# Performance work log

Measured on AMD Instinct MI355X. Metric: run time of the kernel, lower is better.

## Reference

```python
import jax, jax.numpy as jnp
import numpy as np

L, D, DFF, H, B, S = 6, 1024, 4096, 16, 4, 512
DK = D // H
EPS = 1e-6


def setup_inputs() -> dict:
    key = jax.random.key(0)
    ks = jax.random.split(key, 20)
    sc = 0.02
    n = jax.random.normal
    return {
        "x": n(ks[0], (B, S, D), jnp.float32),
        "Wq": n(ks[1], (L, D, D)) * sc, "bq": jnp.zeros((L, D)),
        "Wk": n(ks[2], (L, D, D)) * sc, "bk": jnp.zeros((L, D)),
        "Wv": n(ks[3], (L, D, D)) * sc, "bv": jnp.zeros((L, D)),
        "Wo": n(ks[4], (L, D, D)) * sc, "bo": jnp.zeros((L, D)),
        "W1": n(ks[5], (L, D, DFF)) * sc, "b1": jnp.zeros((L, DFF)),
        "W2": n(ks[6], (L, DFF, D)) * sc, "b2": jnp.zeros((L, D)),
        "ln1_a": jnp.ones((L, D)), "ln1_b": jnp.zeros((L, D)),
        "ln2_a": jnp.ones((L, D)), "ln2_b": jnp.zeros((L, D)),
        "norm_a": jnp.ones((D,)), "norm_b": jnp.zeros((D,)),
    }


def _ln(x, a, b):
    # custom LayerNorm: uses sample std (ddof=1, like torch.std) and (std + eps)
    m = x.mean(-1, keepdims=True)
    s = jnp.std(x, axis=-1, ddof=1, keepdims=True)
    return a * (x - m) / (s + EPS) + b


def reference(x, Wq, bq, Wk, bk, Wv, bv, Wo, bo, W1, b1, W2, b2,
              ln1_a, ln1_b, ln2_a, ln2_b, norm_a, norm_b):
    inv = 1.0 / jnp.sqrt(jnp.float32(DK))
    for l in range(L):
        # --- self-attention sublayer (pre-norm, residual) ---
        h = _ln(x, ln1_a[l], ln1_b[l])
        q = (h @ Wq[l] + bq[l]).reshape(B, S, H, DK)
        k = (h @ Wk[l] + bk[l]).reshape(B, S, H, DK)
        v = (h @ Wv[l] + bv[l]).reshape(B, S, H, DK)
        scores = jnp.einsum('bqhd,bkhd->bhqk', q, k) * inv
        p = jax.nn.softmax(scores, axis=-1)
        o = jnp.einsum('bhqk,bkhd->bqhd', p, v).reshape(B, S, D)
        x = x + (o @ Wo[l] + bo[l])
        # --- feed-forward sublayer ---
        h = _ln(x, ln2_a[l], ln2_b[l])
        x = x + (jax.nn.relu(h @ W1[l] + b1[l]) @ W2[l] + b2[l])
    return _ln(x, norm_a, norm_b)
```

## Files before the change

kernel.cpp:

```cpp
#include <hip/hip_runtime.h>
#include <hip/hip_bf16.h>

typedef __hip_bfloat16 bf16;
typedef __bf16 bf16x8 __attribute__((ext_vector_type(8)));
typedef float f32x4 __attribute__((ext_vector_type(4)));

static constexpr int L_ = 6, D_ = 1024, DFF_ = 4096, H_ = 16, B_ = 4, S_ = 512, DK_ = 64;
static constexpr int N_ = B_ * S_;

#define GLOAD_LDS(gp, lp) __builtin_amdgcn_global_load_lds( \
    (const __attribute__((address_space(1))) void*)(gp),    \
    (__attribute__((address_space(3))) void*)(lp), 16, 0, 0)

__global__ void transpose_cast(const float* __restrict__ in, bf16* __restrict__ out,
                               int K, int M, long zin, long zout) {
    const float* ip = in + (size_t)blockIdx.z * zin;
    bf16* op = out + (size_t)blockIdx.z * zout;
    __shared__ float t[32][33];
    int m0 = blockIdx.x * 32, k0 = blockIdx.y * 32;
    int tx = threadIdx.x, ty = threadIdx.y;
    #pragma unroll
    for (int i = 0; i < 32; i += 8)
        t[ty + i][tx] = ip[(size_t)(k0 + ty + i) * M + m0 + tx];
    __syncthreads();
    #pragma unroll
    for (int i = 0; i < 32; i += 8)
        op[(size_t)(m0 + ty + i) * K + k0 + tx] = __float2bfloat16(t[tx][ty + i]);
}

__global__ void pack_qkv_bias(const float* __restrict__ bq, const float* __restrict__ bk,
                              const float* __restrict__ bv, float* __restrict__ out) {
    int t = blockIdx.x * 256 + threadIdx.x;
    int l = t / (3 * D_), c = t % (3 * D_);
    float v = c < D_ ? bq[l * D_ + c] : (c < 2 * D_ ? bk[l * D_ + c - D_] : bv[l * D_ + c - 2 * D_]);
    out[t] = v;
}

template <typename OutT>
__global__ __launch_bounds__(256) void ln_kernel(const float* __restrict__ x,
                                                 const float* __restrict__ ga,
                                                 const float* __restrict__ gb,
                                                 OutT* __restrict__ out) {
    int row = blockIdx.x;
    float4 v = ((const float4*)(x + (size_t)row * D_))[threadIdx.x];
    float s = v.x + v.y + v.z + v.w;
    float q = v.x * v.x + v.y * v.y + v.z * v.z + v.w * v.w;
    #pragma unroll
    for (int m = 1; m < 64; m <<= 1) { s += __shfl_xor(s, m, 64); q += __shfl_xor(q, m, 64); }
    __shared__ float ps[4], pq[4];
    int wid = threadIdx.x >> 6;
    if ((threadIdx.x & 63) == 0) { ps[wid] = s; pq[wid] = q; }
    __syncthreads();
    s = ps[0] + ps[1] + ps[2] + ps[3];
    q = pq[0] + pq[1] + pq[2] + pq[3];
    float mean = s * (1.0f / D_);
    float var = (q - (float)D_ * mean * mean) * (1.0f / (D_ - 1));
    var = var < 0.f ? 0.f : var;
    float rstd = 1.0f / (sqrtf(var) + 1e-6f);
    int c = threadIdx.x * 4;
    float xv[4] = {v.x, v.y, v.z, v.w};
    #pragma unroll
    for (int r = 0; r < 4; r++) {
        float o = ga[c + r] * (xv[r] - mean) * rstd + gb[c + r];
        if constexpr (__hip_internal::is_same<OutT, float>::value)
            out[(size_t)row * D_ + c + r] = o;
        else
            out[(size_t)row * D_ + c + r] = __float2bfloat16(o);
    }
}

__device__ inline void swz_tiles(int& ntile, int& mtile) {
    unsigned o = blockIdx.y * gridDim.x + blockIdx.x;
    if (gridDim.z == 1) {
        unsigned nwg = gridDim.x * gridDim.y;
        unsigned q = nwg >> 3, r = nwg & 7;
        unsigned xcd = o & 7, j = o >> 3;
        o = (xcd < r ? xcd * (q + 1) : r * (q + 1) + (xcd - r) * q) + j;
    }
    ntile = o % gridDim.x;
    mtile = o / gridDim.x;
}

enum { EPI_RELU = 2, EPI_ATOMIC = 4 };

template <int BM, int BN, int EPI, int SPLITK = 1>
__global__ __launch_bounds__(256) void gemm_bt(
    const bf16* __restrict__ A, int lda,
    const bf16* __restrict__ Bt, int ldb,
    const float* __restrict__ bias,
    void* __restrict__ Cv, int ldc,
    int K) {
    constexpr int BK = 64;
    constexpr int WM = BM / 2, WN = BN / 2;
    constexpr int FM = WM / 16, FN = WN / 16;
    constexpr int IA = BM / 32;
    constexpr int IB = BN / 32;
    __shared__ __align__(16) bf16 As[2][BM * BK];
    __shared__ __align__(16) bf16 Bs[2][BN * BK];
    const int tid = threadIdx.x, wid = tid >> 6, lane = tid & 63;
    const int kz = (SPLITK > 1) ? blockIdx.z : 0;
    int ntile, mtile;
    swz_tiles(ntile, mtile);
    const int m0 = mtile * BM, n0 = ntile * BN;
    const int wm = (wid >> 1) * WM, wn = (wid & 1) * WN;
    const int fr = lane & 15, fg = lane >> 4;
    const int sr = lane >> 3;
    const int c8s = (lane & 7) ^ (sr & 7);
    const int Kc = K / SPLITK;
    const int kbeg = kz * Kc, kend = kbeg + Kc;

    auto stage = [&](int buf, int k0) {
        #pragma unroll
        for (int i = 0; i < IA; i++) {
            int inst = wid * IA + i;
            const bf16* gp = A + (size_t)(m0 + inst * 8 + sr) * lda + k0 + c8s * 8;
            GLOAD_LDS(gp, &As[buf][inst * 512]);
        }
        #pragma unroll
        for (int i = 0; i < IB; i++) {
            int inst = wid * IB + i;
            const bf16* gp = Bt + (size_t)(n0 + inst * 8 + sr) * ldb + k0 + c8s * 8;
            GLOAD_LDS(gp, &Bs[buf][inst * 512]);
        }
    };

    f32x4 acc[FM][FN] = {};
    stage(0, kbeg);
    __syncthreads();
    int cur = 0;
    for (int k0 = kbeg; k0 < kend; k0 += BK) {
        if (k0 + BK < kend) stage(cur ^ 1, k0 + BK);
        #pragma unroll
        for (int kk = 0; kk < 2; kk++) {
            const int cs = ((kk << 2) + fg) ^ (fr & 7);
            bf16x8 af[FM], bfr[FN];
            #pragma unroll
            for (int i = 0; i < FM; i++)
                af[i] = *(const bf16x8*)&As[cur][(wm + i * 16 + fr) * BK + cs * 8];
            #pragma unroll
            for (int j = 0; j < FN; j++)
                bfr[j] = *(const bf16x8*)&Bs[cur][(wn + j * 16 + fr) * BK + cs * 8];
            #pragma unroll
            for (int i = 0; i < FM; i++)
                #pragma unroll
                for (int j = 0; j < FN; j++)
                    acc[i][j] = __builtin_amdgcn_mfma_f32_16x16x32_bf16(af[i], bfr[j], acc[i][j], 0, 0, 0);
        }
        __syncthreads();
        cur ^= 1;
    }
    #pragma unroll
    for (int i = 0; i < FM; i++) {
        #pragma unroll
        for (int j = 0; j < FN; j++) {
            int rr = m0 + wm + i * 16 + (lane >> 4) * 4;
            int cc = n0 + wn + j * 16 + (lane & 15);
            float bv = bias[cc];
            #pragma unroll
            for (int r = 0; r < 4; r++) {
                float v = acc[i][j][r];
                if constexpr (EPI == EPI_RELU) {
                    bf16* C = (bf16*)Cv;
                    float o = v + bv;
                    C[(size_t)(rr + r) * ldc + cc] = __float2bfloat16(o > 0.f ? o : 0.f);
                } else {
                    float* C = (float*)Cv;
                    atomicAdd(&C[(size_t)(rr + r) * ldc + cc], v + (kz == 0 ? bv : 0.f));
                }
            }
        }
    }
}

__global__ __launch_bounds__(256) void gemm_qkv(
    const bf16* __restrict__ A, const bf16* __restrict__ Bt, const float* __restrict__ bias,
    bf16* __restrict__ qb, bf16* __restrict__ kb, bf16* __restrict__ vT) {
    constexpr int BM = 128, BN = 128, BK = 64;
    constexpr int WM = 64, WN = 64, FM = 4, FN = 4;
    __shared__ __align__(16) bf16 As[2][BM * BK];
    __shared__ __align__(16) bf16 Bs[2][BN * BK];
    const int tid = threadIdx.x, wid = tid >> 6, lane = tid & 63;
    int ntile, mtile;
    swz_tiles(ntile, mtile);
    const int m0 = mtile * BM, n0 = ntile * BN;
    const int wm = (wid >> 1) * WM, wn = (wid & 1) * WN;
    const int fr = lane & 15, fg = lane >> 4;
    const int sr = lane >> 3;
    const int c8s = (lane & 7) ^ (sr & 7);

    auto stage = [&](int buf, int k0) {
        #pragma unroll
        for (int i = 0; i < 4; i++) {
            int inst = wid * 4 + i;
            const bf16* gp = A + (size_t)(m0 + inst * 8 + sr) * D_ + k0 + c8s * 8;
            GLOAD_LDS(gp, &As[buf][inst * 512]);
        }
        #pragma unroll
        for (int i = 0; i < 4; i++) {
            int inst = wid * 4 + i;
            const bf16* gp = Bt + (size_t)(n0 + inst * 8 + sr) * D_ + k0 + c8s * 8;
            GLOAD_LDS(gp, &Bs[buf][inst * 512]);
        }
    };

    f32x4 acc[FM][FN] = {};
    stage(0, 0);
    __syncthreads();
    int cur = 0;
    for (int k0 = 0; k0 < D_; k0 += BK) {
        if (k0 + BK < D_) stage(cur ^ 1, k0 + BK);
        #pragma unroll
        for (int kk = 0; kk < 2; kk++) {
            const int cs = ((kk << 2) + fg) ^ (fr & 7);
            bf16x8 af[FM], bfr[FN];
            #pragma unroll
            for (int i = 0; i < FM; i++)
                af[i] = *(const bf16x8*)&As[cur][(wm + i * 16 + fr) * BK + cs * 8];
            #pragma unroll
            for (int j = 0; j < FN; j++)
                bfr[j] = *(const bf16x8*)&Bs[cur][(wn + j * 16 + fr) * BK + cs * 8];
            #pragma unroll
            for (int i = 0; i < FM; i++)
                #pragma unroll
                for (int j = 0; j < FN; j++)
                    acc[i][j] = __builtin_amdgcn_mfma_f32_16x16x32_bf16(af[i], bfr[j], acc[i][j], 0, 0, 0);
        }
        __syncthreads();
        cur ^= 1;
    }
    #pragma unroll
    for (int i = 0; i < FM; i++) {
        #pragma unroll
        for (int j = 0; j < FN; j++) {
            int rr = m0 + wm + i * 16 + (lane >> 4) * 4;
            int cc = n0 + wn + j * 16 + (lane & 15);
            float bv = bias[cc];
            #pragma unroll
            for (int r = 0; r < 4; r++) {
                float v = acc[i][j][r] + bv;
                if (cc < D_) {
                    qb[(size_t)(rr + r) * D_ + cc] = __float2bfloat16(v);
                } else if (cc < 2 * D_) {
                    kb[(size_t)(rr + r) * D_ + cc - D_] = __float2bfloat16(v);
                } else {
                    vT[((size_t)(rr >> 9) * D_ + cc - 2 * D_) * S_ + ((rr & 511) + r)] = __float2bfloat16(v);
                }
            }
        }
    }
}

__global__ __launch_bounds__(256) void flash_attn(
    const bf16* __restrict__ qb, const bf16* __restrict__ kb, const bf16* __restrict__ vT,
    bf16* __restrict__ ob) {
    __shared__ __align__(16) bf16 P[4][16 * 64];
    const int lane = threadIdx.x & 63, wid = threadIdx.x >> 6;
    const int b = blockIdx.y >> 4, h = blockIdx.y & 15;
    const int q0 = blockIdx.x * 64 + wid * 16;
    const int fr = lane & 15, fg = lane >> 4;
    bf16* Pw = &P[wid][0];

    const bf16* qrow = qb + ((size_t)(b * S_ + q0 + fr)) * D_ + h * DK_ + fg * 8;
    bf16x8 aq0 = *(const bf16x8*)(qrow);
    bf16x8 aq1 = *(const bf16x8*)(qrow + 32);

    f32x4 accO[4] = {};
    float mrow[4] = {-1e30f, -1e30f, -1e30f, -1e30f};
    float lrow[4] = {};

    for (int kv0 = 0; kv0 < S_; kv0 += 64) {
        f32x4 s[4] = {};
        #pragma unroll
        for (int j = 0; j < 4; j++) {
            const bf16* krow = kb + ((size_t)(b * S_ + kv0 + j * 16 + fr)) * D_ + h * DK_ + fg * 8;
            bf16x8 bk0 = *(const bf16x8*)(krow);
            bf16x8 bk1 = *(const bf16x8*)(krow + 32);
            s[j] = __builtin_amdgcn_mfma_f32_16x16x32_bf16(aq0, bk0, s[j], 0, 0, 0);
            s[j] = __builtin_amdgcn_mfma_f32_16x16x32_bf16(aq1, bk1, s[j], 0, 0, 0);
        }
        float tmax[4], alpha[4], rs[4];
        #pragma unroll
        for (int r = 0; r < 4; r++) {
            #pragma unroll
            for (int j = 0; j < 4; j++) s[j][r] *= 0.125f;
            tmax[r] = fmaxf(fmaxf(s[0][r], s[1][r]), fmaxf(s[2][r], s[3][r]));
            #pragma unroll
            for (int m = 1; m < 16; m <<= 1) tmax[r] = fmaxf(tmax[r], __shfl_xor(tmax[r], m, 64));
            float mn = fmaxf(mrow[r], tmax[r]);
            alpha[r] = __expf(mrow[r] - mn);
            mrow[r] = mn;
            rs[r] = 0.f;
        }
        #pragma unroll
        for (int j = 0; j < 4; j++) {
            #pragma unroll
            for (int r = 0; r < 4; r++) {
                float p = __expf(s[j][r] - mrow[r]);
                rs[r] += p;
                int q = fg * 4 + r;
                int col = (j * 16 + fr) ^ ((q & 7) << 3);
                Pw[q * 64 + col] = __float2bfloat16(p);
            }
        }
        #pragma unroll
        for (int r = 0; r < 4; r++) {
            #pragma unroll
            for (int m = 1; m < 16; m <<= 1) rs[r] += __shfl_xor(rs[r], m, 64);
            lrow[r] = lrow[r] * alpha[r] + rs[r];
            #pragma unroll
            for (int j = 0; j < 4; j++) accO[j][r] *= alpha[r];
        }
        #pragma unroll
        for (int ks = 0; ks < 2; ks++) {
            int kk = (ks * 32 + fg * 8) ^ ((fr & 7) << 3);
            bf16x8 ap = *(const bf16x8*)&Pw[fr * 64 + kk];
            #pragma unroll
            for (int j = 0; j < 4; j++) {
                const bf16* vrow = vT + ((size_t)(b * D_) + h * DK_ + j * 16 + fr) * S_ + kv0 + ks * 32 + fg * 8;
                bf16x8 bv = *(const bf16x8*)(vrow);
                accO[j] = __builtin_amdgcn_mfma_f32_16x16x32_bf16(ap, bv, accO[j], 0, 0, 0);
            }
        }
    }
    #pragma unroll
    for (int j = 0; j < 4; j++) {
        #pragma unroll
        for (int r = 0; r < 4; r++) {
            int q = q0 + fg * 4 + r;
            int d = h * DK_ + j * 16 + fr;
            ob[(size_t)(b * S_ + q) * D_ + d] = __float2bfloat16(accO[j][r] / lrow[r]);
        }
    }
}

extern "C" void kernel_launch(void* const* d_in, const int* in_sizes, int n_in,
                              void* d_out, int out_size, void* d_ws, size_t ws_size,
                              hipStream_t stream) {
    (void)in_sizes; (void)n_in; (void)out_size;
    const float* x    = (const float*)d_in[0];
    const float* Wq   = (const float*)d_in[1];
    const float* pbq  = (const float*)d_in[2];
    const float* Wk   = (const float*)d_in[3];
    const float* pbk  = (const float*)d_in[4];
    const float* Wv   = (const float*)d_in[5];
    const float* pbv  = (const float*)d_in[6];
    const float* Wo   = (const float*)d_in[7];
    const float* pbo  = (const float*)d_in[8];
    const float* W1   = (const float*)d_in[9];
    const float* pb1  = (const float*)d_in[10];
    const float* W2   = (const float*)d_in[11];
    const float* pb2  = (const float*)d_in[12];
    const float* l1a  = (const float*)d_in[13];
    const float* l1b  = (const float*)d_in[14];
    const float* l2a  = (const float*)d_in[15];
    const float* l2b  = (const float*)d_in[16];
    const float* nrma = (const float*)d_in[17];
    const float* nrmb = (const float*)d_in[18];

    char* ws = (char*)d_ws;
    size_t off = 0;
    auto alloc = [&](size_t bytes) { void* p = ws + off; off += (bytes + 255) & ~(size_t)255; return p; };
    float* xf  = (float*)alloc((size_t)N_ * D_ * 4);
    bf16* hbuf = (bf16*)alloc((size_t)N_ * D_ * 2);
    bf16* qbuf = (bf16*)alloc((size_t)N_ * D_ * 2);
    bf16* kbuf = (bf16*)alloc((size_t)N_ * D_ * 2);
    bf16* vT   = (bf16*)alloc((size_t)B_ * D_ * S_ * 2);
    bf16* obuf = (bf16*)alloc((size_t)N_ * D_ * 2);
    float* qkvb = (float*)alloc((size_t)L_ * 3 * D_ * 4);
    bf16* mid  = (bf16*)alloc((size_t)N_ * DFF_ * 2);
    const size_t szDD = (size_t)D_ * D_, szDF = (size_t)D_ * DFF_;
    size_t wtFull = (3 * L_ * szDD + L_ * szDD + 2 * L_ * szDF) * 2;
    size_t wtLayer = (4 * szDD + 2 * szDF) * 2;
    bool full = (off + wtFull) <= ws_size;
    bf16* WT = (bf16*)alloc(full ? wtFull : wtLayer);

    pack_qkv_bias<<<L_ * 3 * D_ / 256, 256, 0, stream>>>(pbq, pbk, pbv, qkvb);

    bf16 *Wqkv0, *WoT0, *W1T0, *W2T0;
    dim3 tb(32, 8);
    if (full) {
        Wqkv0 = WT;
        WoT0  = WT + 3 * L_ * szDD;
        W1T0  = WoT0 + L_ * szDD;
        W2T0  = W1T0 + L_ * szDF;
        transpose_cast<<<dim3(D_ / 32, D_ / 32, L_), tb, 0, stream>>>(Wq, Wqkv0, D_, D_, szDD, 3 * szDD);
        transpose_cast<<<dim3(D_ / 32, D_ / 32, L_), tb, 0, stream>>>(Wk, Wqkv0 + szDD, D_, D_, szDD, 3 * szDD);
        transpose_cast<<<dim3(D_ / 32, D_ / 32, L_), tb, 0, stream>>>(Wv, Wqkv0 + 2 * szDD, D_, D_, szDD, 3 * szDD);
        transpose_cast<<<dim3(D_ / 32, D_ / 32, L_), tb, 0, stream>>>(Wo, WoT0, D_, D_, szDD, szDD);
        transpose_cast<<<dim3(DFF_ / 32, D_ / 32, L_), tb, 0, stream>>>(W1, W1T0, D_, DFF_, szDF, szDF);
        transpose_cast<<<dim3(D_ / 32, DFF_ / 32, L_), tb, 0, stream>>>(W2, W2T0, DFF_, D_, szDF, szDF);
    } else {
        Wqkv0 = WT; WoT0 = WT + 3 * szDD; W1T0 = WoT0 + szDD; W2T0 = W1T0 + szDF;
    }

    hipMemcpyAsync(xf, x, (size_t)N_ * D_ * 4, hipMemcpyDeviceToDevice, stream);

    for (int l = 0; l < L_; l++) {
        const bf16 *WqkvT, *WoT, *W1T, *W2T;
        if (full) {
            WqkvT = Wqkv0 + (size_t)l * 3 * szDD;
            WoT = WoT0 + l * szDD; W1T = W1T0 + l * szDF; W2T = W2T0 + l * szDF;
        } else {
            transpose_cast<<<dim3(D_ / 32, D_ / 32, 1), tb, 0, stream>>>(Wq + l * szDD, Wqkv0, D_, D_, 0, 0);
            transpose_cast<<<dim3(D_ / 32, D_ / 32, 1), tb, 0, stream>>>(Wk + l * szDD, Wqkv0 + szDD, D_, D_, 0, 0);
            transpose_cast<<<dim3(D_ / 32, D_ / 32, 1), tb, 0, stream>>>(Wv + l * szDD, Wqkv0 + 2 * szDD, D_, D_, 0, 0);
            transpose_cast<<<dim3(D_ / 32, D_ / 32, 1), tb, 0, stream>>>(Wo + l * szDD, WoT0, D_, D_, 0, 0);
            transpose_cast<<<dim3(DFF_ / 32, D_ / 32, 1), tb, 0, stream>>>(W1 + l * szDF, W1T0, D_, DFF_, 0, 0);
            transpose_cast<<<dim3(D_ / 32, DFF_ / 32, 1), tb, 0, stream>>>(W2 + l * szDF, W2T0, DFF_, D_, 0, 0);
            WqkvT = Wqkv0; WoT = WoT0; W1T = W1T0; W2T = W2T0;
        }

        ln_kernel<bf16><<<N_, 256, 0, stream>>>(xf, l1a + l * D_, l1b + l * D_, hbuf);
        gemm_qkv<<<dim3(3 * D_ / 128, N_ / 128, 1), 256, 0, stream>>>(
            hbuf, WqkvT, qkvb + (size_t)l * 3 * D_, qbuf, kbuf, vT);
        flash_attn<<<dim3(S_ / 64, B_ * H_), 256, 0, stream>>>(qbuf, kbuf, vT, obuf);
        gemm_bt<128, 64, EPI_ATOMIC, 2><<<dim3(D_ / 64, N_ / 128, 2), 256, 0, stream>>>(
            obuf, D_, WoT, D_, pbo + l * D_, xf, D_, D_);

        ln_kernel<bf16><<<N_, 256, 0, stream>>>(xf, l2a + l * D_, l2b + l * D_, hbuf);
        gemm_bt<128, 128, EPI_RELU><<<dim3(DFF_ / 128, N_ / 128, 1), 256, 0, stream>>>(
            hbuf, D_, W1T, D_, pb1 + l * DFF_, mid, DFF_, D_);
        gemm_bt<128, 128, EPI_ATOMIC, 4><<<dim3(D_ / 128, N_ / 128, 4), 256, 0, stream>>>(
            mid, DFF_, W2T, DFF_, pb2 + l * D_, xf, D_, DFF_);
    }

    ln_kernel<float><<<N_, 256, 0, stream>>>(xf, nrma, nrmb, (float*)d_out);
}
```

Measured before the change: 1.162 ms.

## Use 256x128 8-wave GEMM, split-K partial buffers, fuse residual reduction with LayerNorm

Replaces the 256-thread GEMMs with one 512-thread kernel using 256x128 tiles for QKV, W1, Wo and W2. Split-K GEMMs now write partial sums to a workspace instead of doing float atomics. A new reduce_ln kernel sums the partials into the residual and applies the next LayerNorm in the same pass, replacing the separate ln_kernel launches. This removes atomic contention and one pass over the activations, at the cost of a 4x N*D fp32 workspace and fewer, larger blocks per GEMM.

```diff
diff --git a/kernel.cpp b/kernel.cpp
--- a/kernel.cpp
+++ b/kernel.cpp
@@ -69,6 +69,44 @@
     }
 }
 
+template <int S, typename OutT>
+__global__ __launch_bounds__(256) void reduce_ln(
+    const float* __restrict__ parts, long sK, float* __restrict__ xf,
+    const float* __restrict__ ga, const float* __restrict__ gb, OutT* __restrict__ out) {
+    int row = blockIdx.x;
+    float4 v = ((const float4*)(xf + (size_t)row * D_))[threadIdx.x];
+    #pragma unroll
+    for (int s = 0; s < S; s++) {
+        float4 p = ((const float4*)(parts + (size_t)s * sK + (size_t)row * D_))[threadIdx.x];
+        v.x += p.x; v.y += p.y; v.z += p.z; v.w += p.w;
+    }
+    ((float4*)(xf + (size_t)row * D_))[threadIdx.x] = v;
+    float sum = v.x + v.y + v.z + v.w;
+    float q = v.x * v.x + v.y * v.y + v.z * v.z + v.w * v.w;
+    #pragma unroll
+    for (int m = 1; m < 64; m <<= 1) { sum += __shfl_xor(sum, m, 64); q += __shfl_xor(q, m, 64); }
+    __shared__ float ps[4], pq[4];
+    int wid = threadIdx.x >> 6;
+    if ((threadIdx.x & 63) == 0) { ps[wid] = sum; pq[wid] = q; }
+    __syncthreads();
+    sum = ps[0] + ps[1] + ps[2] + ps[3];
+    q = pq[0] + pq[1] + pq[2] + pq[3];
+    float mean = sum * (1.0f / D_);
+    float var = (q - (float)D_ * mean * mean) * (1.0f / (D_ - 1));
+    var = var < 0.f ? 0.f : var;
+    float rstd = 1.0f / (sqrtf(var) + 1e-6f);
+    int c = threadIdx.x * 4;
+    float xv[4] = {v.x, v.y, v.z, v.w};
+    #pragma unroll
+    for (int r = 0; r < 4; r++) {
+        float o = ga[c + r] * (xv[r] - mean) * rstd + gb[c + r];
+        if constexpr (__hip_internal::is_same<OutT, float>::value)
+            out[(size_t)row * D_ + c + r] = o;
+        else
+            out[(size_t)row * D_ + c + r] = __float2bfloat16(o);
+    }
+}
+
 __device__ inline void swz_tiles(int& ntile, int& mtile) {
     unsigned o = blockIdx.y * gridDim.x + blockIdx.x;
     if (gridDim.z == 1) {
@@ -81,20 +119,19 @@
     mtile = o / gridDim.x;
 }
 
-enum { EPI_RELU = 2, EPI_ATOMIC = 4 };
-
-template <int BM, int BN, int EPI, int SPLITK = 1>
-__global__ __launch_bounds__(256) void gemm_bt(
+enum { EPI_RELU = 0, EPI_PART = 1, EPI_QKV = 2 };
+
+template <int EPI, int SPLITK = 1>
+__global__ __launch_bounds__(512) void gemm8(
     const bf16* __restrict__ A, int lda,
     const bf16* __restrict__ Bt, int ldb,
     const float* __restrict__ bias,
-    void* __restrict__ Cv, int ldc,
-    int K) {
-    constexpr int BK = 64;
-    constexpr int WM = BM / 2, WN = BN / 2;
-    constexpr int FM = WM / 16, FN = WN / 16;
-    constexpr int IA = BM / 32;
-    constexpr int IB = BN / 32;
+    void* __restrict__ Cv, int ldc, long sK, int K,
+    bf16* __restrict__ qb, bf16* __restrict__ kb, bf16* __restrict__ vT) {
+    constexpr int BM = 256, BN = 128, BK = 64;
+    constexpr int FM = 4, FN = 4;
+    constexpr int IA = BM / 64;
+    constexpr int IB = BN / 64;
     __shared__ __align__(16) bf16 As[2][BM * BK];
     __shared__ __align__(16) bf16 Bs[2][BN * BK];
     const int tid = threadIdx.x, wid = tid >> 6, lane = tid & 63;
@@ -102,7 +139,7 @@
     int ntile, mtile;
     swz_tiles(ntile, mtile);
     const int m0 = mtile * BM, n0 = ntile * BN;
-    const int wm = (wid >> 1) * WM, wn = (wid & 1) * WN;
+    const int wm = (wid >> 1) * 64, wn = (wid & 1) * 64;
     const int fr = lane & 15, fg = lane >> 4;
     const int sr = lane >> 3;
     const int c8s = (lane & 7) ^ (sr & 7);
@@ -163,87 +200,18 @@
                     bf16* C = (bf16*)Cv;
                     float o = v + bv;
                     C[(size_t)(rr + r) * ldc + cc] = __float2bfloat16(o > 0.f ? o : 0.f);
+                } else if constexpr (EPI == EPI_PART) {
+                    float* C = (float*)Cv;
+                    C[(size_t)kz * sK + (size_t)(rr + r) * ldc + cc] = v + (kz == 0 ? bv : 0.f);
                 } else {
-                    float* C = (float*)Cv;
-                    atomicAdd(&C[(size_t)(rr + r) * ldc + cc], v + (kz == 0 ? bv : 0.f));
-                }
-            }
-        }
-    }
-}
-
-__global__ __launch_bounds__(256) void gemm_qkv(
-    const bf16* __restrict__ A, const bf16* __restrict__ Bt, const float* __restrict__ bias,
-    bf16* __restrict__ qb, bf16* __restrict__ kb, bf16* __restrict__ vT) {
-    constexpr int BM = 128, BN = 128, BK = 64;
-    constexpr int WM = 64, WN = 64, FM = 4, FN = 4;
-    __shared__ __align__(16) bf16 As[2][BM * BK];
-    __shared__ __align__(16) bf16 Bs[2][BN * BK];
-    const int tid = threadIdx.x, wid = tid >> 6, lane = tid & 63;
-    int ntile, mtile;
-    swz_tiles(ntile, mtile);
-    const int m0 = mtile * BM, n0 = ntile * BN;
-    const int wm = (wid >> 1) * WM, wn = (wid & 1) * WN;
-    const int fr = lane & 15, fg = lane >> 4;
-    const int sr = lane >> 3;
-    const int c8s = (lane & 7) ^ (sr & 7);
-
-    auto stage = [&](int buf, int k0) {
-        #pragma unroll
-        for (int i = 0; i < 4; i++) {
-            int inst = wid * 4 + i;
-            const bf16* gp = A + (size_t)(m0 + inst * 8 + sr) * D_ + k0 + c8s * 8;
-            GLOAD_LDS(gp, &As[buf][inst * 512]);
-        }
-        #pragma unroll
-        for (int i = 0; i < 4; i++) {
-            int inst = wid * 4 + i;
-            const bf16* gp = Bt + (size_t)(n0 + inst * 8 + sr) * D_ + k0 + c8s * 8;
-            GLOAD_LDS(gp, &Bs[buf][inst * 512]);
-        }
-    };
-
-    f32x4 acc[FM][FN] = {};
-    stage(0, 0);
-    __syncthreads();
-    int cur = 0;
-    for (int k0 = 0; k0 < D_; k0 += BK) {
-        if (k0 + BK < D_) stage(cur ^ 1, k0 + BK);
-        #pragma unroll
-        for (int kk = 0; kk < 2; kk++) {
-            const int cs = ((kk << 2) + fg) ^ (fr & 7);
-            bf16x8 af[FM], bfr[FN];
-            #pragma unroll
-            for (int i = 0; i < FM; i++)
-                af[i] = *(const bf16x8*)&As[cur][(wm + i * 16 + fr) * BK + cs * 8];
-            #pragma unroll
-            for (int j = 0; j < FN; j++)
-                bfr[j] = *(const bf16x8*)&Bs[cur][(wn + j * 16 + fr) * BK + cs * 8];
-            #pragma unroll
-            for (int i = 0; i < FM; i++)
-                #pragma unroll
-                for (int j = 0; j < FN; j++)
-                    acc[i][j] = __builtin_amdgcn_mfma_f32_16x16x32_bf16(af[i], bfr[j], acc[i][j], 0, 0, 0);
-        }
-        __syncthreads();
-        cur ^= 1;
-    }
-    #pragma unroll
-    for (int i = 0; i < FM; i++) {
-        #pragma unroll
-        for (int j = 0; j < FN; j++) {
-            int rr = m0 + wm + i * 16 + (lane >> 4) * 4;
-            int cc = n0 + wn + j * 16 + (lane & 15);
-            float bv = bias[cc];
-            #pragma unroll
-            for (int r = 0; r < 4; r++) {
-                float v = acc[i][j][r] + bv;
-                if (cc < D_) {
-                    qb[(size_t)(rr + r) * D_ + cc] = __float2bfloat16(v);
-                } else if (cc < 2 * D_) {
-                    kb[(size_t)(rr + r) * D_ + cc - D_] = __float2bfloat16(v);
-                } else {
-                    vT[((size_t)(rr >> 9) * D_ + cc - 2 * D_) * S_ + ((rr & 511) + r)] = __float2bfloat16(v);
+                    float o = v + bv;
+                    if (cc < D_) {
+                        qb[(size_t)(rr + r) * D_ + cc] = __float2bfloat16(o);
+                    } else if (cc < 2 * D_) {
+                        kb[(size_t)(rr + r) * D_ + cc - D_] = __float2bfloat16(o);
+                    } else {
+                        vT[((size_t)(rr >> 9) * D_ + cc - 2 * D_) * S_ + ((rr & 511) + r)] = __float2bfloat16(o);
+                    }
                 }
             }
         }
@@ -368,7 +336,9 @@
     bf16* obuf = (bf16*)alloc((size_t)N_ * D_ * 2);
     float* qkvb = (float*)alloc((size_t)L_ * 3 * D_ * 4);
     bf16* mid  = (bf16*)alloc((size_t)N_ * DFF_ * 2);
+    float* wsP = (float*)alloc((size_t)4 * N_ * D_ * 4);
     const size_t szDD = (size_t)D_ * D_, szDF = (size_t)D_ * DFF_;
+    const long sK = (long)N_ * D_;
     size_t wtFull = (3 * L_ * szDD + L_ * szDD + 2 * L_ * szDF) * 2;
     size_t wtLayer = (4 * szDD + 2 * szDF) * 2;
     bool full = (off + wtFull) <= ws_size;
@@ -394,6 +364,7 @@
     }
 
     hipMemcpyAsync(xf, x, (size_t)N_ * D_ * 4, hipMemcpyDeviceToDevice, stream);
+    ln_kernel<bf16><<<N_, 256, 0, stream>>>(xf, l1a, l1b, hbuf);
 
     for (int l = 0; l < L_; l++) {
         const bf16 *WqkvT, *WoT, *W1T, *W2T;
@@ -410,19 +381,19 @@
             WqkvT = Wqkv0; WoT = WoT0; W1T = W1T0; W2T = W2T0;
         }
 
-        ln_kernel<bf16><<<N_, 256, 0, stream>>>(xf, l1a + l * D_, l1b + l * D_, hbuf);
-        gemm_qkv<<<dim3(3 * D_ / 128, N_ / 128, 1), 256, 0, stream>>>(
-            hbuf, WqkvT, qkvb + (size_t)l * 3 * D_, qbuf, kbuf, vT);
+        gemm8<EPI_QKV><<<dim3(3 * D_ / 128, N_ / 256, 1), 512, 0, stream>>>(
+            hbuf, D_, WqkvT, D_, qkvb + (size_t)l * 3 * D_, nullptr, 0, 0, D_, qbuf, kbuf, vT);
         flash_attn<<<dim3(S_ / 64, B_ * H_), 256, 0, stream>>>(qbuf, kbuf, vT, obuf);
-        gemm_bt<128, 64, EPI_ATOMIC, 2><<<dim3(D_ / 64, N_ / 128, 2), 256, 0, stream>>>(
-            obuf, D_, WoT, D_, pbo + l * D_, xf, D_, D_);
-
-        ln_kernel<bf16><<<N_, 256, 0, stream>>>(xf, l2a + l * D_, l2b + l * D_, hbuf);
-        gemm_bt<128, 128, EPI_RELU><<<dim3(DFF_ / 128, N_ / 128, 1), 256, 0, stream>>>(
-            hbuf, D_, W1T, D_, pb1 + l * DFF_, mid, DFF_, D_);
-        gemm_bt<128, 128, EPI_ATOMIC, 4><<<dim3(D_ / 128, N_ / 128, 4), 256, 0, stream>>>(
-            mid, DFF_, W2T, DFF_, pb2 + l * D_, xf, D_, DFF_);
-    }
-
-    ln_kernel<float><<<N_, 256, 0, stream>>>(xf, nrma, nrmb, (float*)d_out);
-}
+        gemm8<EPI_PART, 4><<<dim3(D_ / 128, N_ / 256, 4), 512, 0, stream>>>(
+            obuf, D_, WoT, D_, pbo + l * D_, wsP, D_, sK, D_, nullptr, nullptr, nullptr);
+        reduce_ln<4, bf16><<<N_, 256, 0, stream>>>(wsP, sK, xf, l2a + l * D_, l2b + l * D_, hbuf);
+        gemm8<EPI_RELU><<<dim3(DFF_ / 128, N_ / 256, 1), 512, 0, stream>>>(
+            hbuf, D_, W1T, D_, pb1 + l * DFF_, mid, DFF_, 0, D_, nullptr, nullptr, nullptr);
+        gemm8<EPI_PART, 4><<<dim3(D_ / 128, N_ / 256, 4), 512, 0, stream>>>(
+            mid, DFF_, W2T, DFF_, pb2 + l * D_, wsP, D_, sK, DFF_, nullptr, nullptr, nullptr);
+        if (l < L_ - 1)
+            reduce_ln<4, bf16><<<N_, 256, 0, stream>>>(wsP, sK, xf, l1a + (l + 1) * D_, l1b + (l + 1) * D_, hbuf);
+        else
+            reduce_ln<4, float><<<N_, 256, 0, stream>>>(wsP, sK, xf, nrma, nrmb, (float*)d_out);
+    }
+}
```

Result: no change. 1.161 ms (-0.0%).
